# Optimization experiments

Measured on AMD Instinct MI355X. Metric: run time of the kernel, lower is better.

## Reference

```python
import jax, jax.numpy as jnp
import numpy as np

BETA = 3.0

def setup_inputs() -> dict:
    key = jax.random.key(0)
    k1, k2 = jax.random.split(key)
    B, C = 65536, 1000
    outputs = jax.random.normal(k1, (B, C), dtype=jnp.float32)
    targets = jax.random.randint(k2, (B,), 0, C, dtype=jnp.int64)
    cost_matrix = jnp.zeros((C, C), dtype=jnp.float32)
    return {"outputs": outputs, "targets": targets, "cost_matrix": cost_matrix}

def reference(outputs, targets, cost_matrix):
    # [B, C] log-probs, single stable pass
    log_probs = jax.nn.log_softmax(outputs, axis=1)
    predicted = jnp.argmax(log_probs, axis=1)  # [B]

    # Fused scatter-add replacing the per-sample Python loop:
    # cost_matrix[t, p] += 1 for each (t, p) pair (duplicates accumulate).
    cm = cost_matrix.at[targets, predicted].add(1.0)

    # Row-normalize: cm[i] * beta / max(1, sum(cm[i]))
    row_sum = jnp.sum(cm, axis=1, keepdims=True)  # [C, 1]
    cm_norm = cm * (BETA / jnp.maximum(1.0, row_sum))

    # gather log_probs[b, targets[b]] and cm_norm[targets[b], predicted[b]]
    gather_log_probs = jnp.take_along_axis(log_probs, targets[:, None], axis=1)[:, 0]  # [B]
    gather_costs = cm_norm[targets, predicted]  # [B]

    return -jnp.mean(gather_log_probs * gather_costs)
```

## Files before the change

### kernel.cpp

```cpp
#include <hip/hip_runtime.h>
#include <math.h>

#define CLS 1000
#define VEC_PER_ROW 250
#define BETA 3.0f

__global__ __launch_bounds__(256) void softmax_pass(
    const float* __restrict__ outputs,
    const int* __restrict__ targets,
    float* __restrict__ cm,
    float* __restrict__ logp,
    int* __restrict__ pred,
    int B)
{
    const int wave = threadIdx.x >> 6;
    const int lane = threadIdx.x & 63;
    const int row  = blockIdx.x * 4 + wave;
    if (row >= B) return;

    const float4* rp = (const float4*)(outputs + (size_t)row * CLS);

    float4 r[4];
#pragma unroll
    for (int k = 0; k < 4; ++k) {
        const int j = lane + 64 * k;
        if (j < VEC_PER_ROW) {
            r[k] = rp[j];
        } else {
            r[k] = make_float4(-INFINITY, -INFINITY, -INFINITY, -INFINITY);
        }
    }

    float vmax = -INFINITY;
    int   vidx = 0x7fffffff;
#pragma unroll
    for (int k = 0; k < 4; ++k) {
        const int base = (lane + 64 * k) * 4;
        const float* f = (const float*)&r[k];
#pragma unroll
        for (int c = 0; c < 4; ++c) {
            const float x = f[c];
            if (x > vmax) { vmax = x; vidx = base + c; }
        }
    }

#pragma unroll
    for (int off = 32; off; off >>= 1) {
        const float ov = __shfl_xor(vmax, off);
        const int   oi = __shfl_xor(vidx, off);
        if (ov > vmax || (ov == vmax && oi < vidx)) { vmax = ov; vidx = oi; }
    }

    const int t = targets[row];

    float S  = 0.0f;
    float xt = 0.0f;
#pragma unroll
    for (int k = 0; k < 4; ++k) {
        const int base = (lane + 64 * k) * 4;
        const float* f = (const float*)&r[k];
#pragma unroll
        for (int c = 0; c < 4; ++c) {
            const float x = f[c];
            S += __expf(x - vmax);
            if (base + c == t) xt = x;
        }
    }
#pragma unroll
    for (int off = 32; off; off >>= 1) {
        S  += __shfl_xor(S, off);
        xt += __shfl_xor(xt, off);
    }

    if (lane == 0) {
        logp[row] = xt - vmax - logf(S);
        pred[row] = vidx;
        atomicAdd(&cm[(size_t)t * CLS + vidx], 1.0f);
    }
}

__global__ __launch_bounds__(256) void row_scale(
    const float* __restrict__ cm,
    float* __restrict__ scale)
{
    const int wave = threadIdx.x >> 6;
    const int lane = threadIdx.x & 63;
    const int row  = blockIdx.x * 4 + wave;
    if (row >= CLS) return;

    const float4* rp = (const float4*)(cm + (size_t)row * CLS);
    float s = 0.0f;
    for (int j = lane; j < VEC_PER_ROW; j += 64) {
        const float4 v = rp[j];
        s += v.x + v.y + v.z + v.w;
    }
#pragma unroll
    for (int off = 32; off; off >>= 1) s += __shfl_xor(s, off);
    if (lane == 0) scale[row] = BETA / fmaxf(1.0f, s);
}

__global__ __launch_bounds__(256) void finalize(
    const float* __restrict__ cm,
    const float* __restrict__ scale,
    const float* __restrict__ logp,
    const int* __restrict__ pred,
    const int* __restrict__ targets,
    float* __restrict__ out,
    int B)
{
    const int i = blockIdx.x * 256 + threadIdx.x;
    float v = 0.0f;
    if (i < B) {
        const int t = targets[i];
        const int p = pred[i];
        v = logp[i] * cm[(size_t)t * CLS + p] * scale[t];
    }
    const int lane = threadIdx.x & 63;
    const int wave = threadIdx.x >> 6;
#pragma unroll
    for (int off = 32; off; off >>= 1) v += __shfl_xor(v, off);

    __shared__ float ssum[4];
    if (lane == 0) ssum[wave] = v;
    __syncthreads();
    if (threadIdx.x == 0) {
        const float s = ssum[0] + ssum[1] + ssum[2] + ssum[3];
        atomicAdd(out, -s / (float)B);
    }
}

extern "C" void kernel_launch(void* const* d_in, const int* in_sizes, int n_in,
                              void* d_out, int out_size, void* d_ws, size_t ws_size,
                              hipStream_t stream)
{
    const float* outputs     = (const float*)d_in[0];
    const int*   targets     = (const int*)d_in[1];
    const float* cost_matrix = (const float*)d_in[2];
    const int B = in_sizes[1];

    char* ws = (char*)d_ws;
    float* cm    = (float*)(ws);
    float* logp  = (float*)(ws + 4000000);
    int*   pred  = (int*)  (ws + 4000000 + (size_t)B * 4);
    float* scale = (float*)(ws + 4000000 + (size_t)B * 8);

    hipMemsetAsync(d_out, 0, sizeof(float), stream);
    hipMemcpyAsync(cm, cost_matrix, (size_t)CLS * CLS * sizeof(float),
                   hipMemcpyDeviceToDevice, stream);

    softmax_pass<<<(B + 3) / 4, 256, 0, stream>>>(outputs, targets, cm, logp, pred, B);
    row_scale<<<(CLS + 3) / 4, 256, 0, stream>>>(cm, scale);
    finalize<<<(B + 255) / 256, 256, 0, stream>>>(cm, scale, logp, pred, targets,
                                                  (float*)d_out, B);
}
```

Before: 364.4 us.

## Split max/argmax reductions, fetch target logit directly, two-stage final reduction

```diff
diff --git a/kernel.cpp b/kernel.cpp
--- a/kernel.cpp
+++ b/kernel.cpp
@@ -4,6 +4,7 @@
 #define CLS 1000
 #define VEC_PER_ROW 250
 #define BETA 3.0f
+#define NPART 256
 
 __global__ __launch_bounds__(256) void softmax_pass(
     const float* __restrict__ outputs,
@@ -31,8 +32,16 @@
         }
     }
 
-    float vmax = -INFINITY;
-    int   vidx = 0x7fffffff;
+    float m = -INFINITY;
+#pragma unroll
+    for (int k = 0; k < 4; ++k)
+        m = fmaxf(m, fmaxf(fmaxf(r[k].x, r[k].y), fmaxf(r[k].z, r[k].w)));
+#pragma unroll
+    for (int off = 32; off; off >>= 1)
+        m = fmaxf(m, __shfl_xor(m, off));
+
+    float S  = 0.0f;
+    int  idx = 0x7fffffff;
 #pragma unroll
     for (int k = 0; k < 4; ++k) {
         const int base = (lane + 64 * k) * 4;
@@ -40,42 +49,22 @@
 #pragma unroll
         for (int c = 0; c < 4; ++c) {
             const float x = f[c];
-            if (x > vmax) { vmax = x; vidx = base + c; }
-        }
-    }
-
-#pragma unroll
-    for (int off = 32; off; off >>= 1) {
-        const float ov = __shfl_xor(vmax, off);
-        const int   oi = __shfl_xor(vidx, off);
-        if (ov > vmax || (ov == vmax && oi < vidx)) { vmax = ov; vidx = oi; }
-    }
-
-    const int t = targets[row];
-
-    float S  = 0.0f;
-    float xt = 0.0f;
-#pragma unroll
-    for (int k = 0; k < 4; ++k) {
-        const int base = (lane + 64 * k) * 4;
-        const float* f = (const float*)&r[k];
-#pragma unroll
-        for (int c = 0; c < 4; ++c) {
-            const float x = f[c];
-            S += __expf(x - vmax);
-            if (base + c == t) xt = x;
+            S += __expf(x - m);
+            if (x == m) idx = min(idx, base + c);
         }
     }
 #pragma unroll
     for (int off = 32; off; off >>= 1) {
-        S  += __shfl_xor(S, off);
-        xt += __shfl_xor(xt, off);
+        S   += __shfl_xor(S, off);
+        idx  = min(idx, __shfl_xor(idx, off));
     }
 
     if (lane == 0) {
-        logp[row] = xt - vmax - logf(S);
-        pred[row] = vidx;
-        atomicAdd(&cm[(size_t)t * CLS + vidx], 1.0f);
+        const int t   = targets[row];
+        const float xt = outputs[(size_t)row * CLS + t];
+        logp[row] = xt - m - __logf(S);
+        pred[row] = idx;
+        atomicAdd(&cm[(size_t)t * CLS + idx], 1.0f);
     }
 }
 
@@ -99,21 +88,20 @@
     if (lane == 0) scale[row] = BETA / fmaxf(1.0f, s);
 }
 
-__global__ __launch_bounds__(256) void finalize(
+__global__ __launch_bounds__(256) void finalize_partial(
     const float* __restrict__ cm,
     const float* __restrict__ scale,
     const float* __restrict__ logp,
     const int* __restrict__ pred,
     const int* __restrict__ targets,
-    float* __restrict__ out,
+    float* __restrict__ partial,
     int B)
 {
-    const int i = blockIdx.x * 256 + threadIdx.x;
     float v = 0.0f;
-    if (i < B) {
+    for (int i = blockIdx.x * 256 + threadIdx.x; i < B; i += NPART * 256) {
         const int t = targets[i];
         const int p = pred[i];
-        v = logp[i] * cm[(size_t)t * CLS + p] * scale[t];
+        v += logp[i] * cm[(size_t)t * CLS + p] * scale[t];
     }
     const int lane = threadIdx.x & 63;
     const int wave = threadIdx.x >> 6;
@@ -123,10 +111,26 @@
     __shared__ float ssum[4];
     if (lane == 0) ssum[wave] = v;
     __syncthreads();
-    if (threadIdx.x == 0) {
-        const float s = ssum[0] + ssum[1] + ssum[2] + ssum[3];
-        atomicAdd(out, -s / (float)B);
-    }
+    if (threadIdx.x == 0)
+        partial[blockIdx.x] = ssum[0] + ssum[1] + ssum[2] + ssum[3];
+}
+
+__global__ __launch_bounds__(256) void finalize_reduce(
+    const float* __restrict__ partial,
+    float* __restrict__ out,
+    int B)
+{
+    float v = (threadIdx.x < NPART) ? partial[threadIdx.x] : 0.0f;
+    const int lane = threadIdx.x & 63;
+    const int wave = threadIdx.x >> 6;
+#pragma unroll
+    for (int off = 32; off; off >>= 1) v += __shfl_xor(v, off);
+
+    __shared__ float ssum[4];
+    if (lane == 0) ssum[wave] = v;
+    __syncthreads();
+    if (threadIdx.x == 0)
+        out[0] = -(ssum[0] + ssum[1] + ssum[2] + ssum[3]) / (float)B;
 }
 
 extern "C" void kernel_launch(void* const* d_in, const int* in_sizes, int n_in,
@@ -139,17 +143,18 @@
     const int B = in_sizes[1];
 
     char* ws = (char*)d_ws;
-    float* cm    = (float*)(ws);
-    float* logp  = (float*)(ws + 4000000);
-    int*   pred  = (int*)  (ws + 4000000 + (size_t)B * 4);
-    float* scale = (float*)(ws + 4000000 + (size_t)B * 8);
+    float* cm      = (float*)(ws);
+    float* logp    = (float*)(ws + 4000000);
+    int*   pred    = (int*)  (ws + 4000000 + (size_t)B * 4);
+    float* scale   = (float*)(ws + 4000000 + (size_t)B * 8);
+    float* partial = (float*)(ws + 4000000 + (size_t)B * 8 + 4096);
 
-    hipMemsetAsync(d_out, 0, sizeof(float), stream);
     hipMemcpyAsync(cm, cost_matrix, (size_t)CLS * CLS * sizeof(float),
                    hipMemcpyDeviceToDevice, stream);
 
     softmax_pass<<<(B + 3) / 4, 256, 0, stream>>>(outputs, targets, cm, logp, pred, B);
     row_scale<<<(CLS + 3) / 4, 256, 0, stream>>>(cm, scale);
-    finalize<<<(B + 255) / 256, 256, 0, stream>>>(cm, scale, logp, pred, targets,
-                                                  (float*)d_out, B);
+    finalize_partial<<<NPART, 256, 0, stream>>>(cm, scale, logp, pred, targets,
+                                                partial, B);
+    finalize_reduce<<<1, 256, 0, stream>>>(partial, (float*)d_out, B);
 }
```

New measurement: 361.3 us. Within noise of the previous version (-0.9%).
